# Performance work log

Measured on AMD Instinct MI355X. Metric: run time of the kernel, lower is better.

Reference implementation:

```python
import jax, jax.numpy as jnp
import numpy as np

N = 50000      # nodes
E = 800000     # edges
D = 128        # in_dim == out_dim
H = 8          # heads
DH = D // H    # head dim = 16
BN_EPS = 1e-5


def batch_norm(x, gamma, beta):
    # BatchNorm1d in training mode: biased variance over the node/batch axis.
    mu = jnp.mean(x, axis=0)
    var = jnp.mean((x - mu) ** 2, axis=0)
    return (x - mu) * jax.lax.rsqrt(var + BN_EPS) * gamma + beta


def setup_inputs() -> dict:
    key = jax.random.key(0)
    ks = jax.random.split(key, 16)
    inp = {
        'src': jax.random.randint(ks[0], (E,), 0, N),
        'dst': jax.random.randint(ks[1], (E,), 0, N),
        'h': jax.random.normal(ks[2], (N, D), jnp.float32),
        'e': jax.random.normal(ks[3], (E, D), jnp.float32),
        'h_in': jax.random.normal(ks[4], (N, D), jnp.float32),  # unused: overwritten by h in forward
        # attention projections (bias=False)
        'Wq': jax.random.normal(ks[5], (D, D), jnp.float32) / np.sqrt(D),
        'Wk': jax.random.normal(ks[6], (D, D), jnp.float32) / np.sqrt(D),
        'Wv': jax.random.normal(ks[7], (D, D), jnp.float32) / np.sqrt(D),
        'We': jax.random.normal(ks[8], (D, D), jnp.float32) / np.sqrt(D),
        # sdp_layer (bias=True)
        'W_sdp': jax.random.normal(ks[9], (D, D), jnp.float32) / np.sqrt(D),
        'b_sdp': jnp.zeros((D,), jnp.float32),
        # FFN out_h / out_h_2
        'W_h1': jax.random.normal(ks[10], (D, 2 * D), jnp.float32) / np.sqrt(D),
        'b_h1': jnp.zeros((2 * D,), jnp.float32),
        'W_h2': jax.random.normal(ks[11], (2 * D, D), jnp.float32) / np.sqrt(2 * D),
        'b_h2': jnp.zeros((D,), jnp.float32),
        # batch_norm_1 (shared across both BN applications)
        'bn_gamma': jnp.ones((D,), jnp.float32),
        'bn_beta': jnp.zeros((D,), jnp.float32),
    }
    return inp


def reference(src, dst, h, e, h_in, Wq, Wk, Wv, We, W_sdp, b_sdp,
              W_h1, b_h1, W_h2, b_h2, bn_gamma, bn_beta):
    h_res = h  # h_in = h inside forward

    # --- MultiHeadAttention (default path: all edges real, sum aggregation) ---
    q = (h @ Wq).reshape(N, H, DH)
    k = (h @ Wk).reshape(N, H, DH)
    v = (h @ Wv).reshape(N, H, DH)   # v = v_linear(h_in) with h_in == h
    ef = (e @ We).reshape(E, H, DH)

    # src_dot_dst -> scaling -> imp_exp_attn: elementwise K_src*Q_dst / sqrt(dh) * E
    score = (k[src] * q[dst]) / np.sqrt(DH) * ef          # [E, H, DH]
    # exp('score'): exp(clamp(sum_d score, -5, 5)), keepdim
    score_soft = jnp.exp(jnp.clip(score.sum(-1), -5.0, 5.0))[..., None]  # [E, H, 1]

    aV = jax.ops.segment_sum(v[src] * score_soft, dst, num_segments=N)   # [N, H, DH]
    z = jax.ops.segment_sum(score_soft, dst, num_segments=N)             # [N, H, 1]
    h_attn = (aV / (z + 1e-6)).reshape(N, D)

    # --- EncoderLayer post-attention (dropout=0 -> identity) ---
    hx = h_attn @ W_sdp + b_sdp
    hx = h_res + hx
    hx = batch_norm(hx, bn_gamma, bn_beta)

    h_in2 = hx
    ff = jax.nn.relu(hx @ W_h1 + b_h1) @ W_h2 + b_h2
    hx = h_in2 + ff
    hx = batch_norm(hx, bn_gamma, bn_beta)

    # edge_learning=False: e returned unchanged
    return hx, e
```

## Files before the change

### kernel.cpp

```cpp
#include <hip/hip_runtime.h>
#include <hip/hip_bf16.h>
#include <math.h>

#define N_NODES 50000
#define E_EDGES 800000
#define D_DIM   128
#define H_HEADS 8

typedef __attribute__((ext_vector_type(8))) short short8;
typedef __attribute__((ext_vector_type(4))) float f32x4;
typedef unsigned int   uint_t;
typedef unsigned short ushort_t;

static __device__ __forceinline__ float4 ldg4(const float* p) {
    return *reinterpret_cast<const float4*>(p);
}
static __device__ __forceinline__ ushort_t f2bf(float x) {
    union { float f; uint_t u; } v; v.f = x;
    uint_t r = v.u + 0x7fffu + ((v.u >> 16) & 1u);
    return (ushort_t)(r >> 16);
}
static __device__ __forceinline__ float bf2f(ushort_t b) {
    union { uint_t u; float f; } v; v.u = ((uint_t)b) << 16;
    return v.f;
}
static __device__ __forceinline__ uint_t pk(float lo, float hi) {
    return (uint_t)f2bf(lo) | ((uint_t)f2bf(hi) << 16);
}

__global__ void hist_kernel(const int* __restrict__ dst, int* __restrict__ hist) {
    int i = blockIdx.x * blockDim.x + threadIdx.x;
    if (i < E_EDGES) atomicAdd(&hist[dst[i]], 1);
}

__global__ __launch_bounds__(1024) void scan_kernel(const int* __restrict__ cnt,
                                                    int* __restrict__ start,
                                                    int* __restrict__ cursor) {
    __shared__ int sh[1024];
    const int t = threadIdx.x;
    const int CPT = (N_NODES + 1023) / 1024;
    int lo = t * CPT;
    int hi = lo + CPT; if (hi > N_NODES) hi = N_NODES; if (lo > N_NODES) lo = N_NODES;
    int s = 0;
    for (int i = lo; i < hi; i++) s += cnt[i];
    sh[t] = s;
    __syncthreads();
    for (int off = 1; off < 1024; off <<= 1) {
        int v = (t >= off) ? sh[t - off] : 0;
        __syncthreads();
        sh[t] += v;
        __syncthreads();
    }
    int run = sh[t] - s;
    for (int i = lo; i < hi; i++) {
        start[i]  = run;
        cursor[i] = run;
        run += cnt[i];
    }
    if (t == 1023) start[N_NODES] = sh[1023];
}

__global__ void scatter_kernel(const int* __restrict__ src, const int* __restrict__ dst,
                               int* __restrict__ cursor,
                               int* __restrict__ rank, int* __restrict__ srcs) {
    int i = blockIdx.x * blockDim.x + threadIdx.x;
    if (i < E_EDGES) {
        int p = atomicAdd(&cursor[dst[i]], 1);
        rank[i] = p;
        srcs[p] = src[i];
    }
}

__global__ __launch_bounds__(256) void prep_weights(const float* __restrict__ Wq,
                                                    const float* __restrict__ Wk,
                                                    const float* __restrict__ Wv,
                                                    const float* __restrict__ We,
                                                    const float* __restrict__ Wsdp,
                                                    const float* __restrict__ Wh1,
                                                    const float* __restrict__ Wh2,
                                                    ushort_t* __restrict__ prep) {
    const int b = blockIdx.x;
    const float* W; int ld, cb, kc;
    if (b < 6)       { W = (b < 2 ? Wq : (b < 4 ? Wk : Wv)); ld = 128; cb = 0; kc = b & 1; }
    else if (b < 8)  { W = We;   ld = 128; cb = 0;            kc = b - 6; }
    else if (b < 10) { W = Wsdp; ld = 128; cb = 0;            kc = b - 8; }
    else if (b < 14) { W = Wh1;  ld = 256; cb = (b - 10) >> 1; kc = (b - 10) & 1; }
    else             { W = Wh2;  ld = 128; cb = 0;            kc = b - 14; }
    char* tile = (char*)(prep + (size_t)b * 8192);
    for (int i = threadIdx.x; i < 8192; i += 256) {
        int col = i >> 6, kl = i & 63;
        int k = kc * 64 + kl;
        float v = W[(size_t)k * ld + cb * 128 + col];
        int byte = (col * 128 + kl * 2) ^ ((col & 7) << 4);
        *(ushort_t*)(tile + byte) = f2bf(v);
    }
}

__global__ __launch_bounds__(256) void prep_we_frag(const float* __restrict__ We,
                                                    ushort_t* __restrict__ WeF) {
    int slot = blockIdx.x * 256 + threadIdx.x;
    if (slot < 2048) {
        int lane = slot & 63;
        int kc   = (slot >> 6) & 3;
        int cg   = slot >> 8;
        int col  = cg * 16 + (lane & 15);
        int kb   = kc * 32 + ((lane >> 4) << 3);
#pragma unroll
        for (int j = 0; j < 8; j++)
            WeF[slot * 8 + j] = f2bf(We[(size_t)(kb + j) * 128 + col]);
    }
}

template<int ROWS, int OBF, int ABF, int RBF, int SADD>
__global__ __launch_bounds__(256) void gemm_bf16(const void* __restrict__ Av,
                                                 int M, int K,
                                                 const ushort_t* __restrict__ Bt, int nkc,
                                                 const float* __restrict__ bias,
                                                 const void* __restrict__ residv,
                                                 void* __restrict__ Cv, int ldc,
                                                 size_t cbStride, int doRelu,
                                                 float* __restrict__ sums) {
    constexpr int MI  = ROWS / 32;
    constexpr int TPR = 256 / ROWS;
    constexpr int KPT = 64 / TPR;
    __shared__ __align__(16) unsigned char As[ROWS * 128];
    __shared__ __align__(16) unsigned char Bs[16384];
    __shared__ float csum[128], csq[128];
    const int tid  = threadIdx.x;
    const int lane = tid & 63;
    const int wid  = tid >> 6;
    const int wr   = wid >> 1;
    const int wc   = wid & 1;
    const int cb   = blockIdx.y;
    const int row0 = blockIdx.x * ROWS;

    if (SADD && tid < 128) { csum[tid] = 0.f; csq[tid] = 0.f; }

    f32x4 acc[MI][4];
#pragma unroll
    for (int i = 0; i < MI; i++)
#pragma unroll
        for (int j = 0; j < 4; j++) acc[i][j] = (f32x4){0.f, 0.f, 0.f, 0.f};

    for (int kc = 0; kc < nkc; kc++) {
        __syncthreads();
        {
            int row = tid / TPR;
            int kl0 = (tid % TPR) * KPT;
            int gr  = row0 + row;
            int s = (row & 7) << 4;
            if (ABF) {
                const ushort_t* A16 = (const ushort_t*)Av;
#pragma unroll
                for (int j = 0; j < KPT / 8; j++) {
                    uint4 w = make_uint4(0, 0, 0, 0);
                    if (gr < M) w = *(const uint4*)(&A16[(size_t)gr * K + kc * 64 + kl0 + 8 * j]);
                    int byte = (row * 128 + (kl0 + 8 * j) * 2) ^ s;
                    *(uint4*)(As + byte) = w;
                }
            } else {
                const float* A = (const float*)Av;
                float4 v4[KPT / 4];
                if (gr < M) {
                    const float* ap = &A[(size_t)gr * K + kc * 64 + kl0];
#pragma unroll
                    for (int j = 0; j < KPT / 4; j++) v4[j] = ldg4(ap + 4 * j);
                } else {
#pragma unroll
                    for (int j = 0; j < KPT / 4; j++) v4[j] = make_float4(0.f, 0.f, 0.f, 0.f);
                }
#pragma unroll
                for (int j = 0; j < KPT / 8; j++) {
                    uint4 w;
                    w.x = pk(v4[2 * j].x, v4[2 * j].y);
                    w.y = pk(v4[2 * j].z, v4[2 * j].w);
                    w.z = pk(v4[2 * j + 1].x, v4[2 * j + 1].y);
                    w.w = pk(v4[2 * j + 1].z, v4[2 * j + 1].w);
                    int byte = (row * 128 + (kl0 + 8 * j) * 2) ^ s;
                    *(uint4*)(As + byte) = w;
                }
            }
        }
        {
            const uint4* gB = (const uint4*)(Bt + (size_t)(cb * nkc + kc) * 8192);
#pragma unroll
            for (int j = 0; j < 4; j++) {
                int idx = j * 256 + tid;
                ((uint4*)Bs)[idx] = gB[idx];
            }
        }
        __syncthreads();
#pragma unroll
        for (int k0 = 0; k0 < 64; k0 += 32) {
            short8 a[MI], b[4];
#pragma unroll
            for (int mi = 0; mi < MI; mi++) {
                int row = wr * (ROWS / 2) + mi * 16 + (lane & 15);
                int byte = (row * 128 + k0 * 2 + (lane >> 4) * 16) ^ ((row & 7) << 4);
                a[mi] = *(const short8*)(As + byte);
            }
#pragma unroll
            for (int ni = 0; ni < 4; ni++) {
                int col = wc * 64 + ni * 16 + (lane & 15);
                int byte = (col * 128 + k0 * 2 + (lane >> 4) * 16) ^ ((col & 7) << 4);
                b[ni] = *(const short8*)(Bs + byte);
            }
#pragma unroll
            for (int mi = 0; mi < MI; mi++)
#pragma unroll
                for (int ni = 0; ni < 4; ni++)
                    acc[mi][ni] = __builtin_amdgcn_mfma_f32_16x16x32_bf16(a[mi], b[ni], acc[mi][ni], 0, 0, 0);
        }
    }

    float colS[4] = {0.f, 0.f, 0.f, 0.f};
    float colQ[4] = {0.f, 0.f, 0.f, 0.f};
#pragma unroll
    for (int mi = 0; mi < MI; mi++) {
#pragma unroll
        for (int r = 0; r < 4; r++) {
            int row = row0 + wr * (ROWS / 2) + mi * 16 + ((lane >> 4) << 2) + r;
            if (row < M) {
#pragma unroll
                for (int ni = 0; ni < 4; ni++) {
                    int col = wc * 64 + ni * 16 + (lane & 15);
                    float v = acc[mi][ni][r];
                    if (bias) v += bias[cb * 128 + col];
                    if (doRelu) v = fmaxf(v, 0.f);
                    if (residv) {
                        if (RBF) v += bf2f(((const ushort_t*)residv)[(size_t)row * ldc + col]);
                        else     v += ((const float*)residv)[(size_t)row * ldc + col];
                    }
                    if (SADD) { colS[ni] += v; colQ[ni] += v * v; }
                    if (OBF) ((ushort_t*)Cv)[cb * cbStride + (size_t)row * ldc + col] = f2bf(v);
                    else     ((float*)Cv)[cb * cbStride + (size_t)row * ldc + col] = v;
                }
            }
        }
    }
    if (SADD) {
#pragma unroll
        for (int ni = 0; ni < 4; ni++) {
            int col = wc * 64 + ni * 16 + (lane & 15);
            atomicAdd(&csum[col], colS[ni]);
            atomicAdd(&csq[col],  colQ[ni]);
        }
        __syncthreads();
        if (tid < 128) {
            atomicAdd(&sums[tid],       csum[tid]);
            atomicAdd(&sums[128 + tid], csq[tid]);
        }
    }
}

__global__ __launch_bounds__(512, 8) void edge_mfma(const float* __restrict__ e,
                                                    const int* __restrict__ src,
                                                    const int* __restrict__ dst,
                                                    const ushort_t* __restrict__ Qm,
                                                    const ushort_t* __restrict__ Km,
                                                    const ushort_t* __restrict__ WeF,
                                                    const int* __restrict__ rank,
                                                    float* __restrict__ S,
                                                    float* __restrict__ out_e) {
    __shared__ __align__(16) unsigned char Asm[16384];
    __shared__ float sm[64][8];
    const int tid  = threadIdx.x;
    const int lane = tid & 63;
    const int wid  = tid >> 6;
    const int wr   = wid >> 2;
    const int wc   = wid & 3;
    const int e0   = blockIdx.x * 64;

    {
        int row = tid >> 3;
        int c0  = (tid & 7) * 16;
        const float* ep = &e[(size_t)(e0 + row) * 128 + c0];
        float*       op = &out_e[(size_t)(e0 + row) * 128 + c0];
        float4 v4[4];
#pragma unroll
        for (int j = 0; j < 4; j++) v4[j] = ldg4(ep + 4 * j);
#pragma unroll
        for (int j = 0; j < 4; j++) *(float4*)(op + 4 * j) = v4[j];
        int chunk = c0 >> 6;
        int klb   = (c0 & 63) * 2;
        int s     = (row & 7) << 4;
        uint4 w0, w1;
        w0.x = pk(v4[0].x, v4[0].y); w0.y = pk(v4[0].z, v4[0].w);
        w0.z = pk(v4[1].x, v4[1].y); w0.w = pk(v4[1].z, v4[1].w);
        w1.x = pk(v4[2].x, v4[2].y); w1.y = pk(v4[2].z, v4[2].w);
        w1.z = pk(v4[3].x, v4[3].y); w1.w = pk(v4[3].z, v4[3].w);
        *(uint4*)(Asm + chunk * 8192 + ((row * 128 + klb) ^ s))      = w0;
        *(uint4*)(Asm + chunk * 8192 + ((row * 128 + klb + 16) ^ s)) = w1;
    }
    __syncthreads();

    f32x4 acc[2][2];
#pragma unroll
    for (int i = 0; i < 2; i++)
#pragma unroll
        for (int j = 0; j < 2; j++) acc[i][j] = (f32x4){0.f, 0.f, 0.f, 0.f};

#pragma unroll
    for (int k0 = 0; k0 < 128; k0 += 32) {
        int chunk = k0 >> 6;
        int klb   = (k0 & 63) * 2;
        int kc    = k0 >> 5;
        short8 a[2];
#pragma unroll
        for (int mi = 0; mi < 2; mi++) {
            int arow = wr * 32 + mi * 16 + (lane & 15);
            int byte = chunk * 8192 + ((arow * 128 + klb + (lane >> 4) * 16) ^ ((arow & 7) << 4));
            a[mi] = *(const short8*)(Asm + byte);
        }
#pragma unroll
        for (int ni = 0; ni < 2; ni++) {
            int cg = wc * 2 + ni;
            short8 b = *(const short8*)(WeF + ((size_t)((cg * 4 + kc) * 64 + lane)) * 8);
#pragma unroll
            for (int mi = 0; mi < 2; mi++)
                acc[mi][ni] = __builtin_amdgcn_mfma_f32_16x16x32_bf16(a[mi], b, acc[mi][ni], 0, 0, 0);
        }
    }

#pragma unroll
    for (int mi = 0; mi < 2; mi++) {
        int rows[4], sidx[4], didx[4];
#pragma unroll
        for (int r = 0; r < 4; r++) {
            rows[r] = e0 + wr * 32 + mi * 16 + ((lane >> 4) << 2) + r;
            sidx[r] = src[rows[r]];
            didx[r] = dst[rows[r]];
        }
#pragma unroll
        for (int ni = 0; ni < 2; ni++) {
            int head = wc * 2 + ni;
            int col  = head * 16 + (lane & 15);
            float pv[4];
#pragma unroll
            for (int r = 0; r < 4; r++) {
                float kv = bf2f(Km[(size_t)sidx[r] * 128 + col]);
                float qv = bf2f(Qm[(size_t)didx[r] * 128 + col]);
                pv[r] = acc[mi][ni][r] * kv * qv;
            }
#pragma unroll
            for (int off = 1; off < 16; off <<= 1)
#pragma unroll
                for (int r = 0; r < 4; r++) pv[r] += __shfl_xor(pv[r], off, 64);
            if ((lane & 15) == 0) {
#pragma unroll
                for (int r = 0; r < 4; r++) {
                    float v = fminf(fmaxf(0.25f * pv[r], -5.f), 5.f);
                    sm[rows[r] - e0][head] = __expf(v);
                }
            }
        }
    }
    __syncthreads();
    if (tid < 64) {
        int rk = rank[e0 + tid];
        float4 a0 = *(const float4*)&sm[tid][0];
        float4 a1 = *(const float4*)&sm[tid][4];
        *(float4*)&S[(size_t)rk * 8]     = a0;
        *(float4*)&S[(size_t)rk * 8 + 4] = a1;
    }
}

__global__ __launch_bounds__(256) void agg_kernel(const uint_t* __restrict__ Vu,
                                                  const float* __restrict__ S,
                                                  const int* __restrict__ start,
                                                  const int* __restrict__ srcs,
                                                  uint_t* __restrict__ HAu) {
    const int lane = threadIdx.x & 63;
    const int n = blockIdx.x * 4 + (threadIdx.x >> 6);
    if (n >= N_NODES) return;
    const int s0 = start[n];
    const int s1 = start[n + 1];
    const int h  = lane >> 3;
    float a0 = 0.f, a1 = 0.f, z = 0.f;
    int i = s0;
    for (; i + 4 <= s1; i += 4) {
        int m0 = srcs[i], m1 = srcs[i + 1], m2 = srcs[i + 2], m3 = srcs[i + 3];
        float t0 = S[(size_t)i * 8 + h];
        float t1 = S[(size_t)(i + 1) * 8 + h];
        float t2 = S[(size_t)(i + 2) * 8 + h];
        float t3 = S[(size_t)(i + 3) * 8 + h];
        uint_t v0 = Vu[(size_t)m0 * 64 + lane];
        uint_t v1 = Vu[(size_t)m1 * 64 + lane];
        uint_t v2 = Vu[(size_t)m2 * 64 + lane];
        uint_t v3 = Vu[(size_t)m3 * 64 + lane];
        a0 = fmaf(t0, bf2f((ushort_t)v0), a0); a1 = fmaf(t0, bf2f((ushort_t)(v0 >> 16)), a1);
        a0 = fmaf(t1, bf2f((ushort_t)v1), a0); a1 = fmaf(t1, bf2f((ushort_t)(v1 >> 16)), a1);
        a0 = fmaf(t2, bf2f((ushort_t)v2), a0); a1 = fmaf(t2, bf2f((ushort_t)(v2 >> 16)), a1);
        a0 = fmaf(t3, bf2f((ushort_t)v3), a0); a1 = fmaf(t3, bf2f((ushort_t)(v3 >> 16)), a1);
        z += t0 + t1 + t2 + t3;
    }
    for (; i < s1; i++) {
        int m = srcs[i];
        float t = S[(size_t)i * 8 + h];
        uint_t v = Vu[(size_t)m * 64 + lane];
        a0 = fmaf(t, bf2f((ushort_t)v), a0);
        a1 = fmaf(t, bf2f((ushort_t)(v >> 16)), a1);
        z += t;
    }
    float inv = 1.f / (z + 1e-6f);
    HAu[(size_t)n * 64 + lane] = pk(a0 * inv, a1 * inv);
}

__global__ void bn_finalize(const float* __restrict__ sums,
                            const float* __restrict__ gamma,
                            const float* __restrict__ beta,
                            float* __restrict__ ss) {
    int c = threadIdx.x;
    float mu  = sums[c] * (1.f / (float)N_NODES);
    float var = sums[128 + c] * (1.f / (float)N_NODES) - mu * mu;
    float scale = rsqrtf(var + 1e-5f) * gamma[c];
    ss[c]       = scale;
    ss[128 + c] = beta[c] - mu * scale;
}

template<int OBF>
__global__ __launch_bounds__(256) void bn_apply(const float* __restrict__ X,
                                                const float* __restrict__ ss,
                                                void* __restrict__ Yv) {
    const size_t total = (size_t)N_NODES * 128;
    const size_t step = (size_t)gridDim.x * blockDim.x * 4;
    for (size_t i = ((size_t)blockIdx.x * blockDim.x + threadIdx.x) * 4; i < total; i += step) {
        float4 x = ldg4(&X[i]);
        int c = (int)(i & 127);
        float4 y;
        y.x = x.x * ss[c + 0] + ss[128 + c + 0];
        y.y = x.y * ss[c + 1] + ss[128 + c + 1];
        y.z = x.z * ss[c + 2] + ss[128 + c + 2];
        y.w = x.w * ss[c + 3] + ss[128 + c + 3];
        if (OBF) {
            uint2 p;
            p.x = pk(y.x, y.y);
            p.y = pk(y.z, y.w);
            *(uint2*)((ushort_t*)Yv + i) = p;
        } else {
            *(float4*)((float*)Yv + i) = y;
        }
    }
}

extern "C" void kernel_launch(void* const* d_in, const int* in_sizes, int n_in,
                              void* d_out, int out_size, void* d_ws, size_t ws_size,
                              hipStream_t stream) {
    (void)in_sizes; (void)n_in; (void)out_size; (void)ws_size;
    const int*   src   = (const int*)d_in[0];
    const int*   dst   = (const int*)d_in[1];
    const float* h     = (const float*)d_in[2];
    const float* e     = (const float*)d_in[3];
    const float* Wq    = (const float*)d_in[5];
    const float* Wk    = (const float*)d_in[6];
    const float* Wv    = (const float*)d_in[7];
    const float* We    = (const float*)d_in[8];
    const float* Wsdp  = (const float*)d_in[9];
    const float* bsdp  = (const float*)d_in[10];
    const float* Wh1   = (const float*)d_in[11];
    const float* bh1   = (const float*)d_in[12];
    const float* Wh2   = (const float*)d_in[13];
    const float* bh2   = (const float*)d_in[14];
    const float* gamma = (const float*)d_in[15];
    const float* beta  = (const float*)d_in[16];
    float* out = (float*)d_out;

    float* ws = (float*)d_ws;
    const size_t NM = (size_t)N_NODES * 128;
    ushort_t* Q16  = (ushort_t*)ws;
    ushort_t* K16  = Q16 + NM;
    ushort_t* V16  = Q16 + 2 * NM;
    ushort_t* HA16 = (ushort_t*)(ws + 3 * NM / 2);
    float*    Kb   = ws + 2 * NM;
    float*    Sb   = ws + 3 * NM;
    float*    T1r  = ws + 4 * NM;
    ushort_t* T16  = (ushort_t*)T1r;
    ushort_t* Qb16 = (ushort_t*)(ws + 5 * NM);
    float*    STATS = ws + 6 * NM;
    int* hist   = (int*)(STATS + 1024);
    int* startp = hist + N_NODES;
    int* cursor = startp + N_NODES + 1;
    ushort_t* prep = (ushort_t*)(((uintptr_t)(cursor + N_NODES) + 255) & ~(uintptr_t)255);
    ushort_t* WeF  = prep + (size_t)18 * 8192;

    int* rank = (int*)T1r;
    int* srcs = rank + E_EDGES;

    float* sums1 = STATS;
    float* ss1   = STATS + 256;
    float* sums2 = STATS + 512;
    float* ss2   = STATS + 768;

    prep_weights<<<18, 256, 0, stream>>>(Wq, Wk, Wv, We, Wsdp, Wh1, Wh2, prep);
    prep_we_frag<<<8, 256, 0, stream>>>(We, WeF);

    hipMemsetAsync(STATS, 0, (1024 + N_NODES) * sizeof(float), stream);

    hist_kernel<<<(E_EDGES + 255) / 256, 256, 0, stream>>>(dst, hist);
    scan_kernel<<<1, 1024, 0, stream>>>(hist, startp, cursor);
    scatter_kernel<<<(E_EDGES + 255) / 256, 256, 0, stream>>>(src, dst, cursor, rank, srcs);

    const int rt128 = (N_NODES + 127) / 128;
    const int rt64  = (N_NODES + 63) / 64;

    gemm_bf16<128, 1, 0, 0, 0><<<dim3(rt128, 3), 256, 0, stream>>>(
        h, N_NODES, 128, prep, 2, nullptr, nullptr, Q16, 128, NM, 0, nullptr);

    edge_mfma<<<E_EDGES / 64, 512, 0, stream>>>(e, src, dst, Q16, K16, WeF,
                                                rank, Sb, out + NM);

    agg_kernel<<<(N_NODES + 3) / 4, 256, 0, stream>>>((const uint_t*)V16, Sb, startp, srcs,
                                                      (uint_t*)HA16);

    gemm_bf16<64, 0, 1, 0, 1><<<dim3(rt64, 1), 256, 0, stream>>>(
        HA16, N_NODES, 128, prep + (size_t)8 * 8192, 2, bsdp, h, Kb, 128, 0, 0, sums1);

    bn_finalize<<<1, 128, 0, stream>>>(sums1, gamma, beta, ss1);
    bn_apply<1><<<2048, 256, 0, stream>>>(Kb, ss1, Qb16);

    gemm_bf16<128, 1, 1, 0, 0><<<dim3(rt128, 2), 256, 0, stream>>>(
        Qb16, N_NODES, 128, prep + (size_t)10 * 8192, 2, bh1, nullptr, T16, 256, 128, 1, nullptr);
    gemm_bf16<64, 0, 1, 1, 1><<<dim3(rt64, 1), 256, 0, stream>>>(
        T16, N_NODES, 256, prep + (size_t)14 * 8192, 4, bh2, Qb16, Kb, 128, 0, 0, sums2);

    bn_finalize<<<1, 128, 0, stream>>>(sums2, gamma, beta, ss2);
    bn_apply<0><<<2048, 256, 0, stream>>>(Kb, ss2, out);
}
```

Baseline: 754.6 us.

## Fuse first BatchNorm apply into FFN GEMMs and widen edge_mfma warp tile

The first BatchNorm scale/shift is now applied inside the FFN-1 GEMM's A-tile load and inside the FFN-2 GEMM's residual epilogue, reading the fp32 pre-BN buffer directly. This drops the standalone bn_apply pass and the bf16 normalized intermediate. The edge_mfma kernel is also reshaped from 512 to 256 threads, with each warp computing four heads instead of two. The fused path reads fp32 activations (more bytes than bf16) in FFN-1, and FFN-2 reads and writes the same Kb buffer in place.

```diff
diff --git a/kernel.cpp b/kernel.cpp
--- a/kernel.cpp
+++ b/kernel.cpp
@@ -111,7 +111,7 @@
     }
 }
 
-template<int ROWS, int OBF, int ABF, int RBF, int SADD>
+template<int ROWS, int OBF, int ABF, int RESMODE, int SADD, int ASS>
 __global__ __launch_bounds__(256) void gemm_bf16(const void* __restrict__ Av,
                                                  int M, int K,
                                                  const ushort_t* __restrict__ Bt, int nkc,
@@ -119,7 +119,8 @@
                                                  const void* __restrict__ residv,
                                                  void* __restrict__ Cv, int ldc,
                                                  size_t cbStride, int doRelu,
-                                                 float* __restrict__ sums) {
+                                                 float* __restrict__ sums,
+                                                 const float* __restrict__ ss) {
     constexpr int MI  = ROWS / 32;
     constexpr int TPR = 256 / ROWS;
     constexpr int KPT = 64 / TPR;
@@ -169,6 +170,16 @@
 #pragma unroll
                     for (int j = 0; j < KPT / 4; j++) v4[j] = make_float4(0.f, 0.f, 0.f, 0.f);
                 }
+                if (ASS) {
+#pragma unroll
+                    for (int j = 0; j < KPT / 4; j++) {
+                        int kk = kc * 64 + kl0 + 4 * j;
+                        v4[j].x = v4[j].x * ss[kk + 0] + ss[128 + kk + 0];
+                        v4[j].y = v4[j].y * ss[kk + 1] + ss[128 + kk + 1];
+                        v4[j].z = v4[j].z * ss[kk + 2] + ss[128 + kk + 2];
+                        v4[j].w = v4[j].w * ss[kk + 3] + ss[128 + kk + 3];
+                    }
+                }
 #pragma unroll
                 for (int j = 0; j < KPT / 8; j++) {
                     uint4 w;
@@ -228,8 +239,14 @@
                     if (bias) v += bias[cb * 128 + col];
                     if (doRelu) v = fmaxf(v, 0.f);
                     if (residv) {
-                        if (RBF) v += bf2f(((const ushort_t*)residv)[(size_t)row * ldc + col]);
-                        else     v += ((const float*)residv)[(size_t)row * ldc + col];
+                        if (RESMODE == 1) {
+                            v += bf2f(((const ushort_t*)residv)[(size_t)row * ldc + col]);
+                        } else if (RESMODE == 2) {
+                            float rr = ((const float*)residv)[(size_t)row * ldc + col];
+                            v += rr * ss[col] + ss[128 + col];
+                        } else {
+                            v += ((const float*)residv)[(size_t)row * ldc + col];
+                        }
                     }
                     if (SADD) { colS[ni] += v; colQ[ni] += v * v; }
                     if (OBF) ((ushort_t*)Cv)[cb * cbStride + (size_t)row * ldc + col] = f2bf(v);
@@ -253,7 +270,7 @@
     }
 }
 
-__global__ __launch_bounds__(512, 8) void edge_mfma(const float* __restrict__ e,
+__global__ __launch_bounds__(256, 7) void edge_mfma(const float* __restrict__ e,
                                                     const int* __restrict__ src,
                                                     const int* __restrict__ dst,
                                                     const ushort_t* __restrict__ Qm,
@@ -267,38 +284,42 @@
     const int tid  = threadIdx.x;
     const int lane = tid & 63;
     const int wid  = tid >> 6;
-    const int wr   = wid >> 2;
-    const int wc   = wid & 3;
+    const int wr   = wid >> 1;
+    const int wc   = wid & 1;
     const int e0   = blockIdx.x * 64;
 
     {
-        int row = tid >> 3;
-        int c0  = (tid & 7) * 16;
+        int row = tid >> 2;
+        int c0  = (tid & 3) * 32;
         const float* ep = &e[(size_t)(e0 + row) * 128 + c0];
         float*       op = &out_e[(size_t)(e0 + row) * 128 + c0];
-        float4 v4[4];
-#pragma unroll
-        for (int j = 0; j < 4; j++) v4[j] = ldg4(ep + 4 * j);
-#pragma unroll
-        for (int j = 0; j < 4; j++) *(float4*)(op + 4 * j) = v4[j];
-        int chunk = c0 >> 6;
-        int klb   = (c0 & 63) * 2;
-        int s     = (row & 7) << 4;
-        uint4 w0, w1;
-        w0.x = pk(v4[0].x, v4[0].y); w0.y = pk(v4[0].z, v4[0].w);
-        w0.z = pk(v4[1].x, v4[1].y); w0.w = pk(v4[1].z, v4[1].w);
-        w1.x = pk(v4[2].x, v4[2].y); w1.y = pk(v4[2].z, v4[2].w);
-        w1.z = pk(v4[3].x, v4[3].y); w1.w = pk(v4[3].z, v4[3].w);
-        *(uint4*)(Asm + chunk * 8192 + ((row * 128 + klb) ^ s))      = w0;
-        *(uint4*)(Asm + chunk * 8192 + ((row * 128 + klb + 16) ^ s)) = w1;
+        float4 v4[8];
+#pragma unroll
+        for (int j = 0; j < 8; j++) v4[j] = ldg4(ep + 4 * j);
+#pragma unroll
+        for (int j = 0; j < 8; j++) *(float4*)(op + 4 * j) = v4[j];
+        int s = (row & 7) << 4;
+#pragma unroll
+        for (int g = 0; g < 2; g++) {
+            int cc    = c0 + 16 * g;
+            int chunk = cc >> 6;
+            int klb   = (cc & 63) * 2;
+            uint4 w0, w1;
+            w0.x = pk(v4[4 * g + 0].x, v4[4 * g + 0].y); w0.y = pk(v4[4 * g + 0].z, v4[4 * g + 0].w);
+            w0.z = pk(v4[4 * g + 1].x, v4[4 * g + 1].y); w0.w = pk(v4[4 * g + 1].z, v4[4 * g + 1].w);
+            w1.x = pk(v4[4 * g + 2].x, v4[4 * g + 2].y); w1.y = pk(v4[4 * g + 2].z, v4[4 * g + 2].w);
+            w1.z = pk(v4[4 * g + 3].x, v4[4 * g + 3].y); w1.w = pk(v4[4 * g + 3].z, v4[4 * g + 3].w);
+            *(uint4*)(Asm + chunk * 8192 + ((row * 128 + klb) ^ s))      = w0;
+            *(uint4*)(Asm + chunk * 8192 + ((row * 128 + klb + 16) ^ s)) = w1;
+        }
     }
     __syncthreads();
 
-    f32x4 acc[2][2];
+    f32x4 acc[2][4];
 #pragma unroll
     for (int i = 0; i < 2; i++)
 #pragma unroll
-        for (int j = 0; j < 2; j++) acc[i][j] = (f32x4){0.f, 0.f, 0.f, 0.f};
+        for (int j = 0; j < 4; j++) acc[i][j] = (f32x4){0.f, 0.f, 0.f, 0.f};
 
 #pragma unroll
     for (int k0 = 0; k0 < 128; k0 += 32) {
@@ -313,8 +334,8 @@
             a[mi] = *(const short8*)(Asm + byte);
         }
 #pragma unroll
-        for (int ni = 0; ni < 2; ni++) {
-            int cg = wc * 2 + ni;
+        for (int ni = 0; ni < 4; ni++) {
+            int cg = wc * 4 + ni;
             short8 b = *(const short8*)(WeF + ((size_t)((cg * 4 + kc) * 64 + lane)) * 8);
 #pragma unroll
             for (int mi = 0; mi < 2; mi++)
@@ -332,8 +353,8 @@
             didx[r] = dst[rows[r]];
         }
 #pragma unroll
-        for (int ni = 0; ni < 2; ni++) {
-            int head = wc * 2 + ni;
+        for (int ni = 0; ni < 4; ni++) {
+            int head = wc * 4 + ni;
             int col  = head * 16 + (lane & 15);
             float pv[4];
 #pragma unroll
@@ -418,10 +439,9 @@
     ss[128 + c] = beta[c] - mu * scale;
 }
 
-template<int OBF>
-__global__ __launch_bounds__(256) void bn_apply(const float* __restrict__ X,
-                                                const float* __restrict__ ss,
-                                                void* __restrict__ Yv) {
+__global__ __launch_bounds__(256) void bn_apply_f32(const float* __restrict__ X,
+                                                    const float* __restrict__ ss,
+                                                    float* __restrict__ Y) {
     const size_t total = (size_t)N_NODES * 128;
     const size_t step = (size_t)gridDim.x * blockDim.x * 4;
     for (size_t i = ((size_t)blockIdx.x * blockDim.x + threadIdx.x) * 4; i < total; i += step) {
@@ -432,14 +452,7 @@
         y.y = x.y * ss[c + 1] + ss[128 + c + 1];
         y.z = x.z * ss[c + 2] + ss[128 + c + 2];
         y.w = x.w * ss[c + 3] + ss[128 + c + 3];
-        if (OBF) {
-            uint2 p;
-            p.x = pk(y.x, y.y);
-            p.y = pk(y.z, y.w);
-            *(uint2*)((ushort_t*)Yv + i) = p;
-        } else {
-            *(float4*)((float*)Yv + i) = y;
-        }
+        *(float4*)(&Y[i]) = y;
     }
 }
 
@@ -475,7 +488,6 @@
     float*    Sb   = ws + 3 * NM;
     float*    T1r  = ws + 4 * NM;
     ushort_t* T16  = (ushort_t*)T1r;
-    ushort_t* Qb16 = (ushort_t*)(ws + 5 * NM);
     float*    STATS = ws + 6 * NM;
     int* hist   = (int*)(STATS + 1024);
     int* startp = hist + N_NODES;
@@ -503,26 +515,25 @@
     const int rt128 = (N_NODES + 127) / 128;
     const int rt64  = (N_NODES + 63) / 64;
 
-    gemm_bf16<128, 1, 0, 0, 0><<<dim3(rt128, 3), 256, 0, stream>>>(
-        h, N_NODES, 128, prep, 2, nullptr, nullptr, Q16, 128, NM, 0, nullptr);
-
-    edge_mfma<<<E_EDGES / 64, 512, 0, stream>>>(e, src, dst, Q16, K16, WeF,
+    gemm_bf16<128, 1, 0, 0, 0, 0><<<dim3(rt128, 3), 256, 0, stream>>>(
+        h, N_NODES, 128, prep, 2, nullptr, nullptr, Q16, 128, NM, 0, nullptr, nullptr);
+
+    edge_mfma<<<E_EDGES / 64, 256, 0, stream>>>(e, src, dst, Q16, K16, WeF,
                                                 rank, Sb, out + NM);
 
     agg_kernel<<<(N_NODES + 3) / 4, 256, 0, stream>>>((const uint_t*)V16, Sb, startp, srcs,
                                                       (uint_t*)HA16);
 
-    gemm_bf16<64, 0, 1, 0, 1><<<dim3(rt64, 1), 256, 0, stream>>>(
-        HA16, N_NODES, 128, prep + (size_t)8 * 8192, 2, bsdp, h, Kb, 128, 0, 0, sums1);
+    gemm_bf16<64, 0, 1, 0, 1, 0><<<dim3(rt64, 1), 256, 0, stream>>>(
+        HA16, N_NODES, 128, prep + (size_t)8 * 8192, 2, bsdp, h, Kb, 128, 0, 0, sums1, nullptr);
 
     bn_finalize<<<1, 128, 0, stream>>>(sums1, gamma, beta, ss1);
-    bn_apply<1><<<2048, 256, 0, stream>>>(Kb, ss1, Qb16);
-
-    gemm_bf16<128, 1, 1, 0, 0><<<dim3(rt128, 2), 256, 0, stream>>>(
-        Qb16, N_NODES, 128, prep + (size_t)10 * 8192, 2, bh1, nullptr, T16, 256, 128, 1, nullptr);
-    gemm_bf16<64, 0, 1, 1, 1><<<dim3(rt64, 1), 256, 0, stream>>>(
-        T16, N_NODES, 256, prep + (size_t)14 * 8192, 4, bh2, Qb16, Kb, 128, 0, 0, sums2);
+
+    gemm_bf16<128, 1, 0, 0, 0, 1><<<dim3(rt128, 2), 256, 0, stream>>>(
+        Kb, N_NODES, 128, prep + (size_t)10 * 8192, 2, bh1, nullptr, T16, 256, 128, 1, nullptr, ss1);
+    gemm_bf16<64, 0, 1, 2, 1, 0><<<dim3(rt64, 1), 256, 0, stream>>>(
+        T16, N_NODES, 256, prep + (size_t)14 * 8192, 4, bh2, Kb, Kb, 128, 0, 0, sums2, ss1);
 
     bn_finalize<<<1, 128, 0, stream>>>(sums2, gamma, beta, ss2);
-    bn_apply<0><<<2048, 256, 0, stream>>>(Kb, ss2, out);
-}
+    bn_apply_f32<<<2048, 256, 0, stream>>>(Kb, ss2, out);
+}
```

Result: slower. 837.6 us (+11.0%).
